# Performance work log

Measured on AMD Instinct MI355X. Metric: run time of the kernel, lower is better.

The kernel has to match this reference:

```python
import jax, jax.numpy as jnp
import numpy as np

GROUP = 32  # hadamard_group_size == MXFP4 block size
FP4_GRID = np.array([0.0, 0.5, 1.0, 1.5, 2.0, 3.0, 4.0, 6.0], dtype=np.float32)  # e2m1 magnitudes
FP4_MID = np.array([0.25, 0.75, 1.25, 1.75, 2.5, 3.5, 5.0], dtype=np.float32)    # RTN midpoints


def _hadamard(n):
    # Sylvester construction, normalized so H is orthonormal (matches hadamard(n)*n**-0.5)
    H = np.array([[1.0]], dtype=np.float64)
    while H.shape[0] < n:
        H = np.block([[H, H], [H, -H]])
    return (H / np.sqrt(n)).astype(np.float32)


def _pseudo_quant_mxfp4(t, H, gs):
    """Hadamard-rotate per group of 32, then MXFP4 (e2m1 + power-of-two block scale)
    quant-dequant with abs_max scaling and a global scale. STE through the rounding."""
    shp = t.shape
    rot = t.reshape(-1, GROUP) @ H                      # [n_groups, 32] rotated space
    v = jax.lax.stop_gradient(rot) * gs
    absmax = jnp.max(jnp.abs(v), axis=-1, keepdims=True)
    # E8M0 power-of-two shared scale so that absmax/scale <= 6 (max e2m1 value)
    scale = jnp.exp2(jnp.ceil(jnp.log2(absmax / 6.0 + 1e-30)))
    scale = jnp.where(absmax > 0, scale, 1.0)
    u = v / scale
    grid = jnp.asarray(FP4_GRID)
    mid = jnp.asarray(FP4_MID)
    q = jnp.sign(u) * grid[jnp.searchsorted(mid, jnp.abs(u))]  # round-to-nearest e2m1
    dq = q * scale / gs
    out = rot + jax.lax.stop_gradient(dq - rot)         # straight-through estimator
    return out.reshape(shp)


def setup_inputs() -> dict:
    key = jax.random.key(0)
    kx, kw, kb = jax.random.split(key, 3)
    B, S, K, N = 4, 2048, 4096, 4096
    x = jax.random.normal(kx, (B, S, K), jnp.float32)
    weight = jax.random.normal(kw, (N, K), jnp.float32) * (K ** -0.5)
    bias = jax.random.normal(kb, (N,), jnp.float32)
    H = jnp.asarray(_hadamard(GROUP))
    weight_global_scale = jnp.array([3.0], jnp.float32)  # abs_max method
    act_global_scale = jnp.array([3.0], jnp.float32)
    return {"x": x, "weight": weight, "bias": bias, "hadamard_matrix": H,
            "weight_global_scale": weight_global_scale, "act_global_scale": act_global_scale}


def reference(x, weight, bias, hadamard_matrix, weight_global_scale, act_global_scale):
    x_dq = _pseudo_quant_mxfp4(x, hadamard_matrix, act_global_scale[0])
    w_dq = _pseudo_quant_mxfp4(weight, hadamard_matrix, weight_global_scale[0])
    # both operands stay in the rotated space; per-group Hadamard is orthogonal so
    # x_rot @ w_rot^T == x @ w^T up to quantization error (QuTLASS semantics)
    return jnp.einsum('bsk,nk->bsn', x_dq, w_dq) + bias
```

## Files before the change

kernel.cpp:

```cpp
#include <hip/hip_runtime.h>
#include <hip/hip_bf16.h>

typedef int   i32x4  __attribute__((ext_vector_type(4)));
typedef int   i32x8  __attribute__((ext_vector_type(8)));
typedef float f32x16 __attribute__((ext_vector_type(16)));

__device__ inline void gload_lds16(const void* g, void* l) {
  __builtin_amdgcn_global_load_lds((const __attribute__((address_space(1))) void*)g,
                                   (__attribute__((address_space(3))) void*)l, 16, 0, 0);
}
__device__ inline void gload_lds4(const void* g, void* l) {
  __builtin_amdgcn_global_load_lds((const __attribute__((address_space(1))) void*)g,
                                   (__attribute__((address_space(3))) void*)l, 4, 0, 0);
}
__device__ inline i32x8 pad8(i32x4 v) {
  i32x8 r;
  r[0] = v[0]; r[1] = v[1]; r[2] = v[2]; r[3] = v[3];
  r[4] = 0; r[5] = 0; r[6] = 0; r[7] = 0;
  return r;
}

__global__ __launch_bounds__(256) void quant_fused(const float* __restrict__ x,
                                                   const float* __restrict__ wt,
                                                   unsigned char* __restrict__ xq,
                                                   unsigned char* __restrict__ xsc,
                                                   unsigned char* __restrict__ wq,
                                                   unsigned char* __restrict__ wsc,
                                                   const float* __restrict__ ags,
                                                   const float* __restrict__ wgs,
                                                   int xg, int Mrows, int Nrows, int kg) {
  const int first = blockIdx.x * 256;
  const bool isX = first < xg;
  const float* in        = isX ? x   : wt;
  unsigned char* outq    = isX ? xq  : wq;
  unsigned char* outsc   = isX ? xsc : wsc;
  const float gs         = isX ? ags[0] : wgs[0];
  const int rows         = isX ? Mrows : Nrows;
  const int base         = isX ? first : first - xg;
  const int g = base + threadIdx.x;
  const int r = g / kg, j = g - r * kg;

  float t[32];
  const float4* p4 = (const float4*)(in + (size_t)g * 32);
#pragma unroll
  for (int i = 0; i < 8; ++i) {
    float4 v4 = p4[i];
    t[4 * i + 0] = v4.x; t[4 * i + 1] = v4.y;
    t[4 * i + 2] = v4.z; t[4 * i + 3] = v4.w;
  }
#pragma unroll
  for (int s = 0; s < 5; ++s) {
    const int hh = 1 << s;
#pragma unroll
    for (int i = 0; i < 32; ++i) {
      if ((i & hh) == 0) {
        float a = t[i], b = t[i + hh];
        t[i] = a + b;
        t[i + hh] = a - b;
      }
    }
  }

  const float c = 0.17677669529663687f;
  float v[32];
  float am = 0.0f;
#pragma unroll
  for (int i = 0; i < 32; ++i) {
    float vi = (t[i] * c) * gs;
    v[i] = vi;
    am = fmaxf(am, fabsf(vi));
  }

  float a6 = am / 6.0f;
  int ex;
  float mant = frexpf(a6, &ex);
  int e = (mant == 0.5f) ? ex - 1 : ex;
  if (e < -127) e = -127;
  if (e > 127) e = 127;
  float inv_s = ldexpf(1.0f, -e);

  unsigned int dw[4] = {0u, 0u, 0u, 0u};
#pragma unroll
  for (int i = 0; i < 32; ++i) {
    float u = v[i] * inv_s;
    float au = fabsf(u);
    int idx = (au > 0.25f) + (au > 0.75f) + (au > 1.25f) + (au > 1.75f)
            + (au > 2.5f) + (au > 3.5f) + (au > 5.0f);
    int code = idx | ((u < 0.0f) ? 8 : 0);
    dw[i >> 3] |= (unsigned)code << ((i & 7) * 4);
  }
  i32x4 packed;
  packed[0] = (int)dw[0]; packed[1] = (int)dw[1];
  packed[2] = (int)dw[2]; packed[3] = (int)dw[3];
  *(i32x4*)(outq + (size_t)r * ((size_t)kg * 16) + (size_t)j * 16) = packed;

  int s = j >> 3, j0 = j & 7;
  int p = ((j0 & 1) << 2) | (j0 >> 1);
  if (kg == 128) {
    __shared__ unsigned char sl[256];
    sl[(s << 4) | ((r & 1) << 3) | p] = (unsigned char)(e + 127);
    __syncthreads();
    if (threadIdx.x < 64) {
      int si = threadIdx.x >> 2, wd = threadIdx.x & 3;
      unsigned int vv = *(const unsigned int*)&sl[(si << 4) | (wd << 2)];
      size_t r0 = (size_t)(base / 128);
      *(unsigned int*)(outsc + ((size_t)si * rows + r0) * 8 + (wd << 2)) = vv;
    }
  } else {
    outsc[((size_t)s * rows + r) * 8 + p] = (unsigned char)(e + 127);
  }
}


#define STAGE2(mb, kt, ldsOp) do {                                                   \
    const unsigned char* _s0 = (mb) + (size_t)((w << 4) + (l >> 2)) * KB2            \
                      + (size_t)(kt) * 64 + (size_t)csw * 16;                        \
    gload_lds16(_s0, (unsigned char*)(ldsOp) + (w << 10));                           \
    gload_lds16(_s0 + ((size_t)KB2 << 6), (unsigned char*)(ldsOp) + 4096 + (w << 10)); \
  } while (0)

#define STAGE_ASC(ss, sbuf) gload_lds4(AscG + ((size_t)(ss) * M + brow) * 8 + (tid << 2), \
                                       (unsigned char*)&asc[sbuf][0] + (w << 8))
#define STAGE_BSC(ss, sbuf) gload_lds4(BscG + ((size_t)(ss) * N + bcol) * 8 + (tid << 2), \
                                       (unsigned char*)&bsc[sbuf][0] + (w << 8))

#define LOADB(bf, ssel) do {                                                         \
    const unsigned char* _bb = &lds[bf][1][0];                                       \
    _Pragma("unroll")                                                                \
    for (int nt = 0; nt < 2; ++nt) {                                                 \
      int row = wn * 64 + nt * 32 + (l & 31);                                        \
      int xr = row & 3;                                                              \
      _Pragma("unroll")                                                              \
      for (int kk = 0; kk < 2; ++kk)                                                 \
        bfr[nt][kk] = *(const i32x4*)(_bb + row * 64 + (((kk * 2 + h) ^ xr) << 4));  \
      sb[nt] = *(const int*)((const unsigned char*)&bsc[ssel][0] + row * 8 + h * 4); \
    } } while (0)

#define LOADA(bf, ssel, mt) do {                                                     \
    const unsigned char* _ab = &lds[bf][0][0];                                       \
    int row = wm * 64 + (mt) * 32 + (l & 31);                                        \
    int xr = row & 3;                                                                \
    _Pragma("unroll")                                                                \
    for (int kk = 0; kk < 2; ++kk)                                                   \
      af[kk] = *(const i32x4*)(_ab + row * 64 + (((kk * 2 + h) ^ xr) << 4));         \
    sa = *(const int*)((const unsigned char*)&asc[ssel][0] + row * 8 + h * 4);       \
  } while (0)

#define MF1(mt, nt, kk, OP)                                                          \
  acc[mt][nt] = __builtin_amdgcn_mfma_scale_f32_32x32x64_f8f6f4(                     \
      pad8(af[kk]), pad8(bfr[nt][kk]), acc[mt][nt], 4, 4, OP, sa, OP, sb[nt]);

#define MFMAQ(mt, P) do {                                                            \
    __builtin_amdgcn_s_setprio(1);                                                   \
    MF1(mt, 0, 0, P) MF1(mt, 1, 0, P)                                                \
    MF1(mt, 0, 1, P + 1) MF1(mt, 1, 1, P + 1)                                        \
    __builtin_amdgcn_s_setprio(0);                                                   \
  } while (0)

#define MIDSYNC() do { __builtin_amdgcn_s_barrier();                                 \
    asm volatile("s_waitcnt lgkmcnt(0)" ::: "memory");                               \
    __builtin_amdgcn_sched_barrier(0); } while (0)

#define ENDP() __builtin_amdgcn_s_barrier()
#define VM6()  asm volatile("s_waitcnt vmcnt(6)" ::: "memory")
#define VM4()  asm volatile("s_waitcnt vmcnt(4)" ::: "memory")

__global__ __launch_bounds__(256, 3) void gemm128_fp4(const unsigned char* __restrict__ Aq,
                                                      const unsigned char* __restrict__ Bq,
                                                      const unsigned char* __restrict__ AscG,
                                                      const unsigned char* __restrict__ BscG,
                                                      float* __restrict__ C,
                                                      const float* __restrict__ bias,
                                                      const float* __restrict__ gsx,
                                                      const float* __restrict__ gsw,
                                                      int M, int N, int K) {
  __shared__ __align__(16) unsigned char lds[3][2][8192];
  __shared__ __align__(16) unsigned char asc[2][1024];
  __shared__ __align__(16) unsigned char bsc[2][1024];

  const int tid = threadIdx.x;
  const int w = tid >> 6, l = tid & 63;
  const int wm = w >> 1, wn = w & 1;
  const int h = l >> 5;
  const int csw = (l & 3) ^ ((l >> 2) & 3);
  const int KB2 = K >> 1;

  const int ntn = N >> 7;
  const int nwg = gridDim.x;
  int r_t, c_t;
  {
    int bid = blockIdx.x;
    if ((nwg & 7) == 0) {
      int x = bid & 7, o = bid >> 3, cpx = nwg >> 3;
      int rpx = cpx / ntn;
      if ((ntn & 7) == 0 && rpx > 0 && (cpx % ntn) == 0) {
        int g8 = o & 7, rr = (o >> 3) % rpx, ss = o / (8 * rpx);
        r_t = x * rpx + rr;
        c_t = ss * 8 + g8;
      } else {
        int lin = x * cpx + o;
        r_t = lin / ntn; c_t = lin % ntn;
      }
    } else {
      r_t = bid / ntn; c_t = bid % ntn;
    }
  }
  const size_t brow = (size_t)r_t * 128;
  const size_t bcol = (size_t)c_t * 128;

  const unsigned char* Ab = Aq + brow * (size_t)KB2;
  const unsigned char* Bb = Bq + bcol * (size_t)KB2;

  f32x16 acc[2][2];
#pragma unroll
  for (int m = 0; m < 2; ++m)
#pragma unroll
    for (int n = 0; n < 2; ++n)
#pragma unroll
      for (int r = 0; r < 16; ++r) acc[m][n][r] = 0.0f;

  i32x4 af[2], bfr[2][2];
  int sa, sb[2];

  const int nkt = K / 128;
  const int nss = K / 256;

  STAGE2(Bb, 0, &lds[0][1][0]); STAGE_BSC(0, 0);
  STAGE2(Ab, 0, &lds[0][0][0]); STAGE_ASC(0, 0);
  STAGE2(Bb, 1, &lds[1][1][0]);
  STAGE2(Ab, 1, &lds[1][0][0]);
  VM4();
  __builtin_amdgcn_s_barrier();

  int e = 0, o = 1, n = 2;

  for (int s = 0; s < nkt / 2; ++s) {
    const int t = 2 * s;
    const int t2 = (t + 2 < nkt) ? t + 2 : nkt - 1;
    const int t3 = (t + 3 < nkt) ? t + 3 : nkt - 1;
    const int ssel = s & 1;
    const int ss1 = (s + 1 < nss) ? s + 1 : nss - 1;

    LOADB(e, ssel); LOADA(e, ssel, 0);
    MIDSYNC();
    STAGE2(Bb, t2, &lds[n][1][0]); STAGE_BSC(ss1, ssel ^ 1);
    MFMAQ(0, 0);
    ENDP();
    LOADA(e, ssel, 1);
    MIDSYNC();
    STAGE2(Ab, t2, &lds[n][0][0]); STAGE_ASC(ss1, ssel ^ 1);
    MFMAQ(1, 0);
    VM6();
    ENDP();

    LOADB(o, ssel); LOADA(o, ssel, 0);
    MIDSYNC();
    STAGE2(Bb, t3, &lds[e][1][0]);
    MFMAQ(0, 2);
    ENDP();
    LOADA(o, ssel, 1);
    MIDSYNC();
    STAGE2(Ab, t3, &lds[e][0][0]);
    MFMAQ(1, 2);
    VM4();
    ENDP();

    int tmp = e; e = n; n = o; o = tmp;
  }

  const float inv = 1.0f / (gsx[0] * gsw[0]);
#pragma unroll
  for (int nt = 0; nt < 2; ++nt) {
    const int col = (int)bcol + wn * 64 + nt * 32 + (l & 31);
    const float bv = bias[col];
#pragma unroll
    for (int mt = 0; mt < 2; ++mt) {
      const size_t rbase = brow + (size_t)(wm * 64 + mt * 32 + 4 * h);
#pragma unroll
      for (int r = 0; r < 16; ++r) {
        const size_t row = rbase + (r & 3) + 8 * (r >> 2);
        C[row * (size_t)N + col] = acc[mt][nt][r] * inv + bv;
      }
    }
  }
}

extern "C" void kernel_launch(void* const* d_in, const int* in_sizes, int n_in,
                              void* d_out, int out_size, void* d_ws, size_t ws_size,
                              hipStream_t stream) {
  const float* x    = (const float*)d_in[0];
  const float* wgt  = (const float*)d_in[1];
  const float* bias = (const float*)d_in[2];
  const float* wgs  = (const float*)d_in[4];
  const float* ags  = (const float*)d_in[5];

  const int N = in_sizes[2];
  const int K = in_sizes[1] / N;
  const int M = in_sizes[0] / K;
  const int kg = K / 32;

  unsigned char* aq  = (unsigned char*)d_ws;
  unsigned char* bq  = aq + (size_t)M * (K / 2);
  unsigned char* asc = bq + (size_t)N * (K / 2);
  unsigned char* bsc = asc + (size_t)M * kg;

  const int xg = in_sizes[0] / 32;
  const int wg = in_sizes[1] / 32;
  quant_fused<<<dim3((xg + wg) / 256), dim3(256), 0, stream>>>(
      x, wgt, aq, asc, bq, bsc, ags, wgs, xg, M, N, kg);

  dim3 grid((M / 128) * (N / 128));
  gemm128_fp4<<<grid, dim3(256), 0, stream>>>(aq, bq, asc, bsc, (float*)d_out, bias,
                                              ags, wgs, M, N, K);
}
```

Measured before the change: 166.1 us.

## Switch FP4 GEMM to two-stage double buffering with higher occupancy

```diff
diff --git a/kernel.cpp b/kernel.cpp
--- a/kernel.cpp
+++ b/kernel.cpp
@@ -124,6 +124,11 @@
 #define STAGE_BSC(ss, sbuf) gload_lds4(BscG + ((size_t)(ss) * N + bcol) * 8 + (tid << 2), \
                                        (unsigned char*)&bsc[sbuf][0] + (w << 8))
 
+#define STAGESET(kt, bf) do {                                                        \
+    STAGE2(Bb, kt, &lds[bf][1][0]);                                                  \
+    STAGE2(Ab, kt, &lds[bf][0][0]);                                                  \
+  } while (0)
+
 #define LOADB(bf, ssel) do {                                                         \
     const unsigned char* _bb = &lds[bf][1][0];                                       \
     _Pragma("unroll")                                                                \
@@ -136,36 +141,33 @@
       sb[nt] = *(const int*)((const unsigned char*)&bsc[ssel][0] + row * 8 + h * 4); \
     } } while (0)
 
-#define LOADA(bf, ssel, mt) do {                                                     \
+#define LOADA(bf, ssel) do {                                                         \
     const unsigned char* _ab = &lds[bf][0][0];                                       \
-    int row = wm * 64 + (mt) * 32 + (l & 31);                                        \
-    int xr = row & 3;                                                                \
     _Pragma("unroll")                                                                \
-    for (int kk = 0; kk < 2; ++kk)                                                   \
-      af[kk] = *(const i32x4*)(_ab + row * 64 + (((kk * 2 + h) ^ xr) << 4));         \
-    sa = *(const int*)((const unsigned char*)&asc[ssel][0] + row * 8 + h * 4);       \
-  } while (0)
+    for (int mt = 0; mt < 2; ++mt) {                                                 \
+      int row = wm * 64 + mt * 32 + (l & 31);                                        \
+      int xr = row & 3;                                                              \
+      _Pragma("unroll")                                                              \
+      for (int kk = 0; kk < 2; ++kk)                                                 \
+        af[mt][kk] = *(const i32x4*)(_ab + row * 64 + (((kk * 2 + h) ^ xr) << 4));   \
+      sa[mt] = *(const int*)((const unsigned char*)&asc[ssel][0] + row * 8 + h * 4); \
+    } } while (0)
 
 #define MF1(mt, nt, kk, OP)                                                          \
   acc[mt][nt] = __builtin_amdgcn_mfma_scale_f32_32x32x64_f8f6f4(                     \
-      pad8(af[kk]), pad8(bfr[nt][kk]), acc[mt][nt], 4, 4, OP, sa, OP, sb[nt]);
-
-#define MFMAQ(mt, P) do {                                                            \
+      pad8(af[mt][kk]), pad8(bfr[nt][kk]), acc[mt][nt], 4, 4, OP, sa[mt], OP, sb[nt]);
+
+#define MFMAQ8(P) do {                                                               \
     __builtin_amdgcn_s_setprio(1);                                                   \
-    MF1(mt, 0, 0, P) MF1(mt, 1, 0, P)                                                \
-    MF1(mt, 0, 1, P + 1) MF1(mt, 1, 1, P + 1)                                        \
+    MF1(0, 0, 0, P) MF1(0, 1, 0, P) MF1(1, 0, 0, P) MF1(1, 1, 0, P)                  \
+    MF1(0, 0, 1, P + 1) MF1(0, 1, 1, P + 1) MF1(1, 0, 1, P + 1) MF1(1, 1, 1, P + 1)  \
     __builtin_amdgcn_s_setprio(0);                                                   \
   } while (0)
 
-#define MIDSYNC() do { __builtin_amdgcn_s_barrier();                                 \
-    asm volatile("s_waitcnt lgkmcnt(0)" ::: "memory");                               \
-    __builtin_amdgcn_sched_barrier(0); } while (0)
-
+#define VM0()  asm volatile("s_waitcnt vmcnt(0)" ::: "memory")
 #define ENDP() __builtin_amdgcn_s_barrier()
-#define VM6()  asm volatile("s_waitcnt vmcnt(6)" ::: "memory")
-#define VM4()  asm volatile("s_waitcnt vmcnt(4)" ::: "memory")
-
-__global__ __launch_bounds__(256, 3) void gemm128_fp4(const unsigned char* __restrict__ Aq,
+
+__global__ __launch_bounds__(256, 4) void gemm128_fp4(const unsigned char* __restrict__ Aq,
                                                       const unsigned char* __restrict__ Bq,
                                                       const unsigned char* __restrict__ AscG,
                                                       const unsigned char* __restrict__ BscG,
@@ -174,7 +176,7 @@
                                                       const float* __restrict__ gsx,
                                                       const float* __restrict__ gsw,
                                                       int M, int N, int K) {
-  __shared__ __align__(16) unsigned char lds[3][2][8192];
+  __shared__ __align__(16) unsigned char lds[2][2][8192];
   __shared__ __align__(16) unsigned char asc[2][1024];
   __shared__ __align__(16) unsigned char bsc[2][1024];
 
@@ -219,53 +221,36 @@
 #pragma unroll
       for (int r = 0; r < 16; ++r) acc[m][n][r] = 0.0f;
 
-  i32x4 af[2], bfr[2][2];
-  int sa, sb[2];
+  i32x4 af[2][2], bfr[2][2];
+  int sa[2], sb[2];
 
   const int nkt = K / 128;
   const int nss = K / 256;
 
-  STAGE2(Bb, 0, &lds[0][1][0]); STAGE_BSC(0, 0);
-  STAGE2(Ab, 0, &lds[0][0][0]); STAGE_ASC(0, 0);
-  STAGE2(Bb, 1, &lds[1][1][0]);
-  STAGE2(Ab, 1, &lds[1][0][0]);
-  VM4();
+  STAGESET(0, 0);
+  STAGE_BSC(0, 0); STAGE_ASC(0, 0);
+  VM0();
   __builtin_amdgcn_s_barrier();
-
-  int e = 0, o = 1, n = 2;
 
   for (int s = 0; s < nkt / 2; ++s) {
     const int t = 2 * s;
+    const int t1 = t + 1;
     const int t2 = (t + 2 < nkt) ? t + 2 : nkt - 1;
-    const int t3 = (t + 3 < nkt) ? t + 3 : nkt - 1;
     const int ssel = s & 1;
     const int ss1 = (s + 1 < nss) ? s + 1 : nss - 1;
 
-    LOADB(e, ssel); LOADA(e, ssel, 0);
-    MIDSYNC();
-    STAGE2(Bb, t2, &lds[n][1][0]); STAGE_BSC(ss1, ssel ^ 1);
-    MFMAQ(0, 0);
+    STAGESET(t1, 1);
+    STAGE_BSC(ss1, ssel ^ 1); STAGE_ASC(ss1, ssel ^ 1);
+    LOADB(0, ssel); LOADA(0, ssel);
+    MFMAQ8(0);
+    VM0();
     ENDP();
-    LOADA(e, ssel, 1);
-    MIDSYNC();
-    STAGE2(Ab, t2, &lds[n][0][0]); STAGE_ASC(ss1, ssel ^ 1);
-    MFMAQ(1, 0);
-    VM6();
+
+    STAGESET(t2, 0);
+    LOADB(1, ssel); LOADA(1, ssel);
+    MFMAQ8(2);
+    VM0();
     ENDP();
-
-    LOADB(o, ssel); LOADA(o, ssel, 0);
-    MIDSYNC();
-    STAGE2(Bb, t3, &lds[e][1][0]);
-    MFMAQ(0, 2);
-    ENDP();
-    LOADA(o, ssel, 1);
-    MIDSYNC();
-    STAGE2(Ab, t3, &lds[e][0][0]);
-    MFMAQ(1, 2);
-    VM4();
-    ENDP();
-
-    int tmp = e; e = n; n = o; o = tmp;
   }
 
   const float inv = 1.0f / (gsx[0] * gsw[0]);
```

After: 218.8 us. +31.8%, slower.
